# Optimization experiments

Measured on AMD Instinct MI355X. Metric: run time of the kernel, lower is better.

Reference implementation:

```python
import jax, jax.numpy as jnp
import numpy as np

B, T, D, H, O = 128, 1024, 256, 512, 256

def setup_inputs() -> dict:
    key = jax.random.key(0)
    k0, k1, k2, k3 = jax.random.split(key, 4)
    s_i = 1.0 / np.sqrt(D)
    s_h = 1.0 / np.sqrt(H)
    return {
        "X": jax.random.normal(k0, (B, T, D), jnp.float32),
        "Wi": jax.random.normal(k1, (D, 4 * H), jnp.float32) * s_i,  # input kernel (no bias in flax OptimizedLSTMCell input dense)
        "Wh": jax.random.normal(k2, (H, 4 * H), jnp.float32) * s_h,  # recurrent kernel
        "b": jnp.zeros((4 * H,), jnp.float32),                        # recurrent bias
        "Wd": jax.random.normal(k3, (H, O), jnp.float32) * s_h,      # output Dense kernel
        "bd": jnp.zeros((O,), jnp.float32),                           # output Dense bias
    }

def _lstm_last_hidden(X, Wi, Wh, b):
    # Precompute input projections for all timesteps (same linear map, hoisted out of scan)
    x_proj = jnp.einsum('btd,dg->btg', X, Wi)  # [B, T, 4H]
    h_dim = Wh.shape[0]
    c0 = jnp.zeros((X.shape[0], h_dim), X.dtype)
    h0 = c0

    def step(carry, xt):
        c, h = carry
        y = xt + h @ Wh + b  # [B, 4H]
        i, f, g, o = jnp.split(y, 4, axis=-1)  # flax OptimizedLSTMCell gate order: i, f, g, o
        i = jax.nn.sigmoid(i)
        f = jax.nn.sigmoid(f)
        g = jnp.tanh(g)
        o = jax.nn.sigmoid(o)
        c_new = f * c + i * g
        h_new = o * jnp.tanh(c_new)
        return (c_new, h_new), None

    (c_T, h_T), _ = jax.lax.scan(step, (c0, h0), jnp.swapaxes(x_proj, 0, 1))
    return h_T  # [B, H] = last hidden state

def reference(X, Wi, Wh, b, Wd, bd):
    # Original applies Dense to all timesteps then slices [:, -1, :];
    # Dense is pointwise over time, so applying it to the last hidden is identical math.
    h_last = _lstm_last_hidden(X, Wi, Wh, b)
    return h_last @ Wd + bd  # [B, O]
```

## Files before the change

kernel.cpp:

```cpp
#include <hip/hip_runtime.h>
#include <hip/hip_bf16.h>

#define Bb 128
#define Tt 1024
#define Dd 256
#define Hh 512
#define G4 2048
#define Oo 256

#define NBG 8
#define WPB 16
#define NWG_LAUNCH 256
#define BLOCK 512

#define SPIN_CAP (1u << 20)

typedef __attribute__((ext_vector_type(8))) short short8;
typedef __attribute__((ext_vector_type(4))) float f32x4;
typedef unsigned long long u64;

#define TICK_OFF 0
#define CNT_OFF  2048
#define HBUF_OFF 4096
#define WS_ZERO_BYTES (4096 + Bb*Hh*2)

__device__ __forceinline__ short f2bf(float f) {
  __hip_bfloat16 h = __float2bfloat16(f);
  return *reinterpret_cast<short*>(&h);
}
__device__ __forceinline__ float sigm(float x) {
  return __builtin_amdgcn_rcpf(1.f + __expf(-x));
}
__device__ __forceinline__ float tanh_(float x) {
  return fmaf(2.f, __builtin_amdgcn_rcpf(1.f + __expf(-2.f * x)), -1.f);
}

#define MFMA16(A, B, C) __builtin_amdgcn_mfma_f32_16x16x32_bf16((A), (B), (C), 0, 0, 0)

__global__ __launch_bounds__(BLOCK, 2) void lstm_seq(
    const float* __restrict__ X, const float* __restrict__ Wi,
    const float* __restrict__ Wh, const float* __restrict__ bias,
    char* hbuf, int* cnts, int* tickets)
{
  __shared__ char sH[16 * 1024];
  __shared__ char sX[16 * 512];
  __shared__ unsigned short hstage[16][40];
  __shared__ int sSlot;

  const int tid  = threadIdx.x;
  const int w    = tid >> 6;
  const int lane = tid & 63;

  int myxcc;
  asm volatile("s_getreg_b32 %0, hwreg(HW_REG_XCC_ID)" : "=s"(myxcc));
  myxcc &= 7;
  if (tid == 0) {
    sSlot = __hip_atomic_fetch_add(&tickets[myxcc * 16], 1,
                                   __ATOMIC_RELAXED, __HIP_MEMORY_SCOPE_AGENT);
  }
  __syncthreads();
  const int gjw = sSlot;
  if (gjw >= WPB) return;
  const int bg = myxcc;
  int* cnt = cnts + bg * 32;

  const int cjj  = lane & 15;
  const int kgrp = lane >> 4;
  const int gate = cjj >> 2;
  const int c4   = cjj & 3;
  const int colg = gate * Hh + gjw * 32 + w * 4 + c4;

  short8 wf[24];
#pragma unroll
  for (int kk = 0; kk < 24; ++kk) {
    short8 f;
#pragma unroll
    for (int i = 0; i < 8; ++i) {
      int k = kk * 32 + kgrp * 8 + i;
      float v = (k < Hh) ? Wh[(size_t)k * G4 + colg]
                         : Wi[(size_t)(k - Hh) * G4 + colg];
      f[i] = f2bf(v);
    }
    wf[kk] = f;
  }
  const float bvv = bias[colg];

  const int arow = cjj;
  const int aswz = (arow & 7) << 4;
  float cpr[4] = {0.f, 0.f, 0.f, 0.f};

  for (int s = 1; s <= Tt; ++s) {
    const char* hread  = hbuf + (size_t)((s - 1) & 1) * (Bb * Hh * 2);
    char*       hwrite = hbuf + (size_t)(s & 1) * (Bb * Hh * 2);

    {
      int row = tid >> 5, seg = tid & 31;
      const float* xp = X + ((size_t)(bg * 16 + row) * Tt + (s - 1)) * Dd + seg * 8;
      f32x4 x0 = *reinterpret_cast<const f32x4*>(xp);
      f32x4 x1 = *reinterpret_cast<const f32x4*>(xp + 4);
      short8 xb;
      xb[0] = f2bf(x0[0]); xb[1] = f2bf(x0[1]); xb[2] = f2bf(x0[2]); xb[3] = f2bf(x0[3]);
      xb[4] = f2bf(x1[0]); xb[5] = f2bf(x1[1]); xb[6] = f2bf(x1[2]); xb[7] = f2bf(x1[3]);
      *reinterpret_cast<short8*>(sX + row * 512 + ((seg * 16) ^ ((row & 7) << 4))) = xb;
    }

    if (s > 1 && tid == 0) {
      const int tgt = WPB * (s - 1);
      unsigned spin = 0;
      while ((int)(__hip_atomic_fetch_add((unsigned*)cnt, 0x10000u,
                                          __ATOMIC_RELAXED,
                                          __HIP_MEMORY_SCOPE_WORKGROUP) & 0xFFFFu) < tgt
             && ++spin < SPIN_CAP) {}
    }
    __syncthreads();

    asm volatile("buffer_inv sc0" ::: "memory");
#pragma unroll
    for (int q = 0; q < 2; ++q) {
      int c = tid + q * 512, row = c >> 6, off = c & 63;
      f32x4 v = *reinterpret_cast<const f32x4*>(
          hread + (size_t)(bg * 16 + row) * 1024 + off * 16);
      *reinterpret_cast<f32x4*>(sH + row * 1024 + ((off * 16) ^ ((row & 7) << 4))) = v;
    }
    __syncthreads();

    f32x4 acc;
#pragma unroll
    for (int m = 0; m < 4; ++m) acc[m] = bvv;
#pragma unroll
    for (int kk = 0; kk < 16; ++kk) {
      short8 a = *reinterpret_cast<const short8*>(
          sH + arow * 1024 + ((kk * 64 + kgrp * 16) ^ aswz));
      acc = MFMA16(a, wf[kk], acc);
    }
#pragma unroll
    for (int kk = 0; kk < 8; ++kk) {
      short8 a = *reinterpret_cast<const short8*>(
          sX + arow * 512 + ((kk * 64 + kgrp * 16) ^ aswz));
      acc = MFMA16(a, wf[16 + kk], acc);
    }

    float r1[4], r2[4], r3[4];
#pragma unroll
    for (int m = 0; m < 4; ++m) {
      r1[m] = __shfl_xor(acc[m], 4);
      r2[m] = __shfl_xor(acc[m], 8);
      r3[m] = __shfl_xor(r1[m], 8);
    }
    if (cjj < 4) {
#pragma unroll
      for (int m = 0; m < 4; ++m) {
        float ig = sigm(acc[m]), fg = sigm(r1[m]);
        float gg = tanh_(r2[m]), og = sigm(r3[m]);
        float c = fg * cpr[m] + ig * gg;
        cpr[m] = c;
        float hh = og * tanh_(c);
        __hip_bfloat16 hb = __float2bfloat16(hh);
        hstage[kgrp * 4 + m][w * 4 + c4] = *reinterpret_cast<unsigned short*>(&hb);
      }
    }
    __syncthreads();

    if (tid < 64) {
      int row = tid >> 2, chunk = tid & 3;
      f32x4 v = *reinterpret_cast<const f32x4*>(&hstage[row][chunk * 8]);
      *reinterpret_cast<f32x4*>(
          hwrite + ((size_t)(bg * 16 + row) * Hh + gjw * 32 + chunk * 8) * 2) = v;
    }
    __syncthreads();

    if (tid == 0) {
      (void)__hip_atomic_fetch_add(cnt, 1, __ATOMIC_RELAXED,
                                   __HIP_MEMORY_SCOPE_WORKGROUP);
    }
  }
}

__global__ void out_dense(const __hip_bfloat16* __restrict__ hT,
                          const float* __restrict__ Wd,
                          const float* __restrict__ bd,
                          float* __restrict__ out)
{
  __shared__ float hrow[Hh];
  int b = blockIdx.x;
  int o = threadIdx.x;
  for (int k = o; k < Hh; k += Oo)
    hrow[k] = __bfloat162float(hT[(size_t)b * Hh + k]);
  __syncthreads();
  float acc = bd[o];
  for (int k = 0; k < Hh; ++k)
    acc = fmaf(hrow[k], Wd[(size_t)k * Oo + o], acc);
  out[(size_t)b * Oo + o] = acc;
}

extern "C" void kernel_launch(void* const* d_in, const int* in_sizes, int n_in,
                              void* d_out, int out_size, void* d_ws, size_t ws_size,
                              hipStream_t stream) {
  (void)in_sizes; (void)n_in; (void)out_size; (void)ws_size;
  const float* X  = (const float*)d_in[0];
  const float* Wi = (const float*)d_in[1];
  const float* Wh = (const float*)d_in[2];
  const float* b  = (const float*)d_in[3];
  const float* Wd = (const float*)d_in[4];
  const float* bd = (const float*)d_in[5];
  float* out = (float*)d_out;

  char* ws = (char*)d_ws;
  int* tickets = (int*)(ws + TICK_OFF);
  int* cnts    = (int*)(ws + CNT_OFF);
  char* hbuf   = ws + HBUF_OFF;

  hipMemsetAsync(d_ws, 0, WS_ZERO_BYTES, stream);
  lstm_seq<<<NWG_LAUNCH, BLOCK, 0, stream>>>(X, Wi, Wh, b, hbuf, cnts, tickets);
  out_dense<<<Bb, Oo, 0, stream>>>((const __hip_bfloat16*)hbuf, Wd, bd, out);
}
```

Baseline: 2.685 ms.

## Prefetch X two steps ahead, split MFMA accumulators, sleep in spin-wait

The per-step X loads for a timestep are now issued two steps early into double-buffered registers, so global load latency overlaps the previous steps' barrier and compute. The dependent MFMA chain is split into two independent accumulators that are summed at the end, which shortens the dependency chain. The spin-wait loop gains an s_sleep and a lower spin cap, which reduces atomic pressure but can add wake-up latency to the cross-workgroup barrier. A lower cap also makes an early exit without synchronization more likely under contention.

```diff
diff --git a/kernel.cpp b/kernel.cpp
--- a/kernel.cpp
+++ b/kernel.cpp
@@ -13,7 +13,7 @@
 #define NWG_LAUNCH 256
 #define BLOCK 512
 
-#define SPIN_CAP (1u << 20)
+#define SPIN_CAP (1u << 16)
 
 typedef __attribute__((ext_vector_type(8))) short short8;
 typedef __attribute__((ext_vector_type(4))) float f32x4;
@@ -89,19 +89,22 @@
   const int aswz = (arow & 7) << 4;
   float cpr[4] = {0.f, 0.f, 0.f, 0.f};
 
-  for (int s = 1; s <= Tt; ++s) {
+  const int xrow = tid >> 5, xseg = tid & 31;
+  const float* xbase = X + (size_t)(bg * 16 + xrow) * Tt * Dd + xseg * 8;
+  f32x4 xA0 = *reinterpret_cast<const f32x4*>(xbase);
+  f32x4 xA1 = *reinterpret_cast<const f32x4*>(xbase + 4);
+  f32x4 xB0 = *reinterpret_cast<const f32x4*>(xbase + Dd);
+  f32x4 xB1 = *reinterpret_cast<const f32x4*>(xbase + Dd + 4);
+
+  auto STEP = [&](int s, f32x4& xv0, f32x4& xv1) {
     const char* hread  = hbuf + (size_t)((s - 1) & 1) * (Bb * Hh * 2);
     char*       hwrite = hbuf + (size_t)(s & 1) * (Bb * Hh * 2);
 
     {
-      int row = tid >> 5, seg = tid & 31;
-      const float* xp = X + ((size_t)(bg * 16 + row) * Tt + (s - 1)) * Dd + seg * 8;
-      f32x4 x0 = *reinterpret_cast<const f32x4*>(xp);
-      f32x4 x1 = *reinterpret_cast<const f32x4*>(xp + 4);
       short8 xb;
-      xb[0] = f2bf(x0[0]); xb[1] = f2bf(x0[1]); xb[2] = f2bf(x0[2]); xb[3] = f2bf(x0[3]);
-      xb[4] = f2bf(x1[0]); xb[5] = f2bf(x1[1]); xb[6] = f2bf(x1[2]); xb[7] = f2bf(x1[3]);
-      *reinterpret_cast<short8*>(sX + row * 512 + ((seg * 16) ^ ((row & 7) << 4))) = xb;
+      xb[0] = f2bf(xv0[0]); xb[1] = f2bf(xv0[1]); xb[2] = f2bf(xv0[2]); xb[3] = f2bf(xv0[3]);
+      xb[4] = f2bf(xv1[0]); xb[5] = f2bf(xv1[1]); xb[6] = f2bf(xv1[2]); xb[7] = f2bf(xv1[3]);
+      *reinterpret_cast<short8*>(sX + xrow * 512 + ((xseg * 16) ^ ((xrow & 7) << 4))) = xb;
     }
 
     if (s > 1 && tid == 0) {
@@ -110,7 +113,9 @@
       while ((int)(__hip_atomic_fetch_add((unsigned*)cnt, 0x10000u,
                                           __ATOMIC_RELAXED,
                                           __HIP_MEMORY_SCOPE_WORKGROUP) & 0xFFFFu) < tgt
-             && ++spin < SPIN_CAP) {}
+             && ++spin < SPIN_CAP) {
+        __builtin_amdgcn_s_sleep(2);
+      }
     }
     __syncthreads();
 
@@ -124,21 +129,36 @@
     }
     __syncthreads();
 
+    f32x4 acc_a, acc_b;
+#pragma unroll
+    for (int m = 0; m < 4; ++m) { acc_a[m] = bvv; acc_b[m] = 0.f; }
+#pragma unroll
+    for (int kk = 0; kk < 8; ++kk) {
+      short8 a = *reinterpret_cast<const short8*>(
+          sH + arow * 1024 + ((kk * 64 + kgrp * 16) ^ aswz));
+      acc_a = MFMA16(a, wf[kk], acc_a);
+    }
+#pragma unroll
+    for (int kk = 8; kk < 16; ++kk) {
+      short8 a = *reinterpret_cast<const short8*>(
+          sH + arow * 1024 + ((kk * 64 + kgrp * 16) ^ aswz));
+      acc_b = MFMA16(a, wf[kk], acc_b);
+    }
+#pragma unroll
+    for (int kk = 0; kk < 4; ++kk) {
+      short8 a = *reinterpret_cast<const short8*>(
+          sX + arow * 512 + ((kk * 64 + kgrp * 16) ^ aswz));
+      acc_a = MFMA16(a, wf[16 + kk], acc_a);
+    }
+#pragma unroll
+    for (int kk = 4; kk < 8; ++kk) {
+      short8 a = *reinterpret_cast<const short8*>(
+          sX + arow * 512 + ((kk * 64 + kgrp * 16) ^ aswz));
+      acc_b = MFMA16(a, wf[16 + kk], acc_b);
+    }
     f32x4 acc;
 #pragma unroll
-    for (int m = 0; m < 4; ++m) acc[m] = bvv;
-#pragma unroll
-    for (int kk = 0; kk < 16; ++kk) {
-      short8 a = *reinterpret_cast<const short8*>(
-          sH + arow * 1024 + ((kk * 64 + kgrp * 16) ^ aswz));
-      acc = MFMA16(a, wf[kk], acc);
-    }
-#pragma unroll
-    for (int kk = 0; kk < 8; ++kk) {
-      short8 a = *reinterpret_cast<const short8*>(
-          sX + arow * 512 + ((kk * 64 + kgrp * 16) ^ aswz));
-      acc = MFMA16(a, wf[16 + kk], acc);
-    }
+    for (int m = 0; m < 4; ++m) acc[m] = acc_a[m] + acc_b[m];
 
     float r1[4], r2[4], r3[4];
 #pragma unroll
@@ -173,6 +193,16 @@
       (void)__hip_atomic_fetch_add(cnt, 1, __ATOMIC_RELAXED,
                                    __HIP_MEMORY_SCOPE_WORKGROUP);
     }
+
+    if (s + 2 <= Tt) {
+      xv0 = *reinterpret_cast<const f32x4*>(xbase + (size_t)(s + 1) * Dd);
+      xv1 = *reinterpret_cast<const f32x4*>(xbase + (size_t)(s + 1) * Dd + 4);
+    }
+  };
+
+  for (int s = 1; s <= Tt; s += 2) {
+    STEP(s,     xA0, xA1);
+    STEP(s + 1, xB0, xB1);
   }
 }
 
```

New measurement: 2.659 ms. Within noise of the previous version (-1.0%).
